# Performance work log

Hardware: AMD Instinct MI355X
Metric: run time of the kernel (lower is better)

Reference implementation:

```python
import jax, jax.numpy as jnp
import numpy as np

INF_SUB_NUM = -9000000000000000.0
LN_EPS = 1e-5


def _layernorm(x, gamma, beta):
    mu = jnp.mean(x, axis=-1, keepdims=True)
    var = jnp.mean(jnp.square(x - mu), axis=-1, keepdims=True)
    return gamma * (x - mu) * jax.lax.rsqrt(var + LN_EPS) + beta


def setup_inputs() -> dict:
    key = jax.random.key(0)
    kh, ke, kt, kw1, kw2 = jax.random.split(key, 5)
    B, N, E, D = 8, 4096, 2048, 256
    stdv = 1.0 / np.sqrt(D)
    return {
        "hidden": jax.random.normal(kh, (B, N, D), dtype=jnp.float32),
        "ht": jax.random.randint(kt, (B, E, N), 0, 2, dtype=jnp.int32),
        "edge_emb": jax.random.normal(ke, (B, E, D), dtype=jnp.float32),
        "wnk": jax.random.uniform(kw1, (D, D), jnp.float32, -stdv, stdv),
        "wek": jax.random.uniform(kw2, (D, D), jnp.float32, -stdv, stdv),
        "ln_gamma": jnp.ones((D,), jnp.float32),
        "ln_beta": jnp.zeros((D,), jnp.float32),
    }


def reference(hidden, ht, edge_emb, wnk, wek, ln_gamma, ln_beta):
    # hidden: [B,N,D]; ht: [B,E,N] incidence; edge_emb: [B,E,D]
    D = hidden.shape[-1]
    scale = 1.0 / jnp.sqrt(jnp.float32(D))

    edge_emb = _layernorm(edge_emb, ln_gamma, ln_beta)          # [B,E,D]
    node_k = hidden @ wnk                                        # [B,N,D]

    # Stage 1: edges attend over their incident nodes (softmax over N, dim=2)
    edge_scores = jnp.einsum('bed,bnd->ben', edge_emb, node_k) * scale
    edge_scores = jnp.where(ht > 0, edge_scores, INF_SUB_NUM)
    attn_edge = jax.nn.softmax(edge_scores, axis=2)              # [B,E,N]
    edge_h = jnp.einsum('ben,bnd->bed', attn_edge, hidden) + edge_emb

    # Stage 2: nodes gather from edges; softmax over N (dim=1), as in source
    edge_k = edge_h @ wek                                        # [B,E,D]
    node_scores = jnp.einsum('bnd,bed->bne', node_k, edge_k) * scale
    node_scores = jnp.where(jnp.transpose(ht, (0, 2, 1)) > 0, node_scores, INF_SUB_NUM)
    attn_node = jax.nn.softmax(node_scores, axis=1)              # [B,N,E]
    node_hidden = jnp.einsum('bne,bed->bnd', attn_node, edge_h)  # [B,N,D]
    return node_hidden
```

## Files before the change

### kernel.cpp

```cpp
#include <hip/hip_runtime.h>
#include <hip/hip_bf16.h>
#include <stdint.h>


#define B_ 8
#define N_ 4096
#define E_ 2048
#define D_ 256
#define INF_SUB (-9.0e15f)

typedef short bf16x8 __attribute__((ext_vector_type(8)));
typedef float f32x4 __attribute__((ext_vector_type(4)));
typedef unsigned short us8 __attribute__((ext_vector_type(8)));

#define AS1 __attribute__((address_space(1)))
#define AS3 __attribute__((address_space(3)))

__device__ __forceinline__ unsigned short f2bf(float f) {
    union { float f; unsigned int u; } v; v.f = f;
    unsigned int r = v.u + 0x7fffu + ((v.u >> 16) & 1u);
    return (unsigned short)(r >> 16);
}
__device__ __forceinline__ float bf2f(unsigned short h) {
    union { unsigned int u; float f; } v; v.u = ((unsigned int)h) << 16;
    return v.f;
}
__device__ __forceinline__ float waveReduceSum(float v) {
#pragma unroll
    for (int o = 32; o > 0; o >>= 1) v += __shfl_xor(v, o, 64);
    return v;
}

__global__ __launch_bounds__(256) void ln_kernel(const float* __restrict__ x,
                                                 const float* __restrict__ gamma,
                                                 const float* __restrict__ beta,
                                                 unsigned short* __restrict__ yb) {
    __shared__ float red[8];
    const int row = blockIdx.x;
    const int t = threadIdx.x;
    const int lane = t & 63, wid = t >> 6;
    const float v = x[(size_t)row * D_ + t];
    float s = waveReduceSum(v);
    if (lane == 0) red[wid] = s;
    __syncthreads();
    const float mu = (red[0] + red[1] + red[2] + red[3]) * (1.0f / D_);
    const float d = v - mu;
    float s2 = waveReduceSum(d * d);
    if (lane == 0) red[4 + wid] = s2;
    __syncthreads();
    const float var = (red[4] + red[5] + red[6] + red[7]) * (1.0f / D_);
    yb[(size_t)row * D_ + t] = f2bf(gamma[t] * d * rsqrtf(var + 1e-5f) + beta[t]);
}

__global__ __launch_bounds__(256) void pack_mask(const int* __restrict__ ht,
                                                 uint32_t* __restrict__ bits) {
    const int row = blockIdx.x;
    const int t = threadIdx.x, wid = t >> 6, lane = t & 63;
    const int* hrow = ht + (size_t)row * N_;
    uint32_t* brow = bits + (size_t)row * (N_ / 32);
#pragma unroll
    for (int i = 0; i < 16; ++i) {
        const int c = wid * 16 + i;
        const int v = hrow[c * 64 + lane];
        unsigned long long m = __ballot(v > 0);
        if (lane == 0) {
            brow[c * 2] = (uint32_t)m;
            brow[c * 2 + 1] = (uint32_t)(m >> 32);
        }
    }
}

__global__ __launch_bounds__(256) void prep_hidden(const float* __restrict__ in,
                                                   unsigned short* __restrict__ hb,
                                                   unsigned short* __restrict__ hT) {
    __shared__ unsigned short tile[64][65];
    const int b = blockIdx.z;
    in += (size_t)b * N_ * D_;
    hb += (size_t)b * N_ * D_;
    hT += (size_t)b * D_ * N_;
    const int n0 = blockIdx.y * 64, d0 = blockIdx.x * 64;
    const int t = threadIdx.x;
    const int tr = t >> 4, tc = (t & 15) * 4;
#pragma unroll
    for (int q = 0; q < 4; ++q) {
        const int rr = q * 16 + tr;
        const float4 f = *(const float4*)&in[(size_t)(n0 + rr) * D_ + d0 + tc];
        unsigned short h0 = f2bf(f.x), h1 = f2bf(f.y), h2 = f2bf(f.z), h3 = f2bf(f.w);
        *(ushort4*)&hb[(size_t)(n0 + rr) * D_ + d0 + tc] = make_ushort4(h0, h1, h2, h3);
        tile[rr][tc + 0] = h0; tile[rr][tc + 1] = h1;
        tile[rr][tc + 2] = h2; tile[rr][tc + 3] = h3;
    }
    __syncthreads();
#pragma unroll
    for (int q = 0; q < 4; ++q) {
        const int cc = q * 16 + tr;
        ushort4 o = make_ushort4(tile[tc + 0][cc], tile[tc + 1][cc],
                                 tile[tc + 2][cc], tile[tc + 3][cc]);
        *(ushort4*)&hT[(size_t)(d0 + cc) * N_ + n0 + tc] = o;
    }
}

__global__ __launch_bounds__(256) void cast_wT(const float* __restrict__ w,
                                               unsigned short* __restrict__ wT) {
    const int gid = blockIdx.x * 256 + threadIdx.x;
    const int i = gid >> 8, j = gid & 255;
    wT[j * D_ + i] = f2bf(w[i * D_ + j]);
}

__global__ __launch_bounds__(256) void reduce_pv(const float* __restrict__ slab,
                                                 const unsigned short* __restrict__ eln,
                                                 const float* __restrict__ rsum,
                                                 unsigned short* __restrict__ eh,
                                                 float* __restrict__ ehT) {
    __shared__ float tile[64][65];
    const int b = blockIdx.z;
    const float* s0 = slab + (size_t)(b * 2) * E_ * D_;
    const float* s1 = slab + (size_t)(b * 2 + 1) * E_ * D_;
    const int e0 = blockIdx.y * 64, d0 = blockIdx.x * 64;
    const int t = threadIdx.x;
    const int tr = t >> 4, tc = (t & 15) * 4;
#pragma unroll
    for (int q = 0; q < 4; ++q) {
        const int rr = q * 16 + tr;
        const int row = e0 + rr;
        const float4 v0 = *(const float4*)&s0[(size_t)row * D_ + d0 + tc];
        const float4 v1 = *(const float4*)&s1[(size_t)row * D_ + d0 + tc];
        const float inv = 1.0f / rsum[(size_t)b * E_ + row];
        const ushort4 el = *(const ushort4*)&eln[(size_t)b * E_ * D_ + (size_t)row * D_ + d0 + tc];
        const float x0 = (v0.x + v1.x) * inv + bf2f(el.x);
        const float x1 = (v0.y + v1.y) * inv + bf2f(el.y);
        const float x2 = (v0.z + v1.z) * inv + bf2f(el.z);
        const float x3 = (v0.w + v1.w) * inv + bf2f(el.w);
        *(ushort4*)&eh[(size_t)b * E_ * D_ + (size_t)row * D_ + d0 + tc] =
            make_ushort4(f2bf(x0), f2bf(x1), f2bf(x2), f2bf(x3));
        tile[rr][tc + 0] = x0; tile[rr][tc + 1] = x1;
        tile[rr][tc + 2] = x2; tile[rr][tc + 3] = x3;
    }
    __syncthreads();
#pragma unroll
    for (int q = 0; q < 4; ++q) {
        const int cc = q * 16 + tr;
        float4 o = make_float4(tile[tc + 0][cc], tile[tc + 1][cc],
                               tile[tc + 2][cc], tile[tc + 3][cc]);
        *(float4*)&ehT[(size_t)b * D_ * E_ + (size_t)(d0 + cc) * E_ + e0 + tc] = o;
    }
}

__global__ __launch_bounds__(256) void scale_ehT(const float* __restrict__ ehT,
                                                 const float* __restrict__ lsum,
                                                 unsigned short* __restrict__ ehs) {
    const size_t base = ((size_t)blockIdx.x * 256 + threadIdx.x) * 8;
    const int b = (int)(base / ((size_t)D_ * E_));
    const int e = (int)(base % E_);
    const float4 f0 = *(const float4*)&ehT[base];
    const float4 f1 = *(const float4*)&ehT[base + 4];
    const float4 l0 = *(const float4*)&lsum[(size_t)b * E_ + e];
    const float4 l1 = *(const float4*)&lsum[(size_t)b * E_ + e + 4];
    us8 o;
    o[0] = f2bf(f0.x / l0.x); o[1] = f2bf(f0.y / l0.y);
    o[2] = f2bf(f0.z / l0.z); o[3] = f2bf(f0.w / l0.w);
    o[4] = f2bf(f1.x / l1.x); o[5] = f2bf(f1.y / l1.y);
    o[6] = f2bf(f1.z / l1.z); o[7] = f2bf(f1.w / l1.w);
    *(us8*)&ehs[base] = o;
}

#define M_BF16 0
#define M_MASK 1
#define M_F32 2

template <int MODE, int MASKOR, int AEXP, int ASUM, int SPLIT, int CSUM>
__global__ __launch_bounds__(256) void mfma_gemm_nt(
        const short* __restrict__ A, const short* __restrict__ Bm,
        void* __restrict__ Cv, const uint32_t* __restrict__ bits,
        float* __restrict__ sums,
        int K, int ldc, size_t sA, size_t sB, size_t sC, float scale) {
    __shared__ __align__(16) short ls[(MODE == M_F32) ? 16384 : 16896];
    __shared__ uint32_t mwords[MASKOR ? 512 : 4];
    short* lsA = ls;
    short* lsB = ls + 8192;
    const int zb = blockIdx.z;
    const int b = SPLIT ? (zb >> 1) : zb;
    A += (size_t)b * sA;
    Bm += (size_t)b * sB;
    const int m0 = blockIdx.y * 128, n0 = blockIdx.x * 128;
    const int tid = threadIdx.x, wid = tid >> 6, lane = tid & 63;
    const int l15 = lane & 15, kg = lane >> 4;
    const int wr = wid >> 1, wc = wid & 1;

    if (MASKOR) {
        const uint32_t* bb = bits + (size_t)b * E_ * (N_ / 32);
#pragma unroll
        for (int q = 0; q < 2; ++q) {
            const int idx = q * 256 + tid;
            mwords[idx] = (MASKOR == 1)
                ? bb[(size_t)(m0 + (idx >> 2)) * (N_ / 32) + (n0 >> 5) + (idx & 3)]
                : bb[(size_t)(n0 + (idx >> 2)) * (N_ / 32) + (m0 >> 5) + (idx & 3)];
        }
    }

    int raoff[4], rota[4], rboff[4], rotb[4];
#pragma unroll
    for (int i = 0; i < 4; ++i) {
        const int ra = wr * 64 + i * 16 + l15;
        raoff[i] = ra * 64; rota[i] = kg + (ra >> 1);
        const int rb = wc * 64 + i * 16 + l15;
        rboff[i] = rb * 64; rotb[i] = kg + (rb >> 1);
    }
    const f32x4 zero = {0.f, 0.f, 0.f, 0.f};
    f32x4 acc[4][4];
#pragma unroll
    for (int i = 0; i < 4; ++i)
#pragma unroll
        for (int j = 0; j < 4; ++j) acc[i][j] = zero;

    float rsumLoc = 0.f;
    const int ar = tid >> 1, ah = tid & 1;

    const int kt0 = SPLIT ? (zb & 1) * (K >> 1) : 0;
    const int ktE = SPLIT ? kt0 + (K >> 1) : K;
    for (int kt = kt0; kt < ktE; kt += 64) {
        __syncthreads();
        if (AEXP) {
            const short* ga = A + (size_t)(m0 + ar) * K + kt + ah * 32;
            us8 raw[4], ex[4];
#pragma unroll
            for (int c = 0; c < 4; ++c) raw[c] = *(const us8*)(ga + c * 8);
#pragma unroll
            for (int c = 0; c < 4; ++c)
#pragma unroll
                for (int j = 0; j < 8; ++j) {
                    const float x = __expf(bf2f(raw[c][j]));
                    if (ASUM) rsumLoc += x;
                    ex[c][j] = f2bf(x);
                }
#pragma unroll
            for (int c = 0; c < 4; ++c) {
                const int p = (ah * 4 + c + (ar >> 1)) & 7;
                *(us8*)&lsA[ar * 64 + p * 8] = ex[c];
            }
#pragma unroll
            for (int q = 0; q < 4; ++q) {
                const int c = q * 256 + tid;
                const int r = c >> 3;
                const int kc = ((c & 7) - (r >> 1)) & 7;
                const short* gb = Bm + (size_t)(n0 + r) * K + kt + kc * 8;
                __builtin_amdgcn_global_load_lds((const AS1 void*)gb,
                    (AS3 void*)(lsB + (q * 256 + wid * 64) * 8), 16, 0, 0);
            }
        } else {
#pragma unroll
            for (int q = 0; q < 4; ++q) {
                const int c = q * 256 + tid;
                const int r = c >> 3;
                const int kc = ((c & 7) - (r >> 1)) & 7;
                const short* ga = A + (size_t)(m0 + r) * K + kt + kc * 8;
                __builtin_amdgcn_global_load_lds((const AS1 void*)ga,
                    (AS3 void*)(lsA + (q * 256 + wid * 64) * 8), 16, 0, 0);
                const short* gb = Bm + (size_t)(n0 + r) * K + kt + kc * 8;
                __builtin_amdgcn_global_load_lds((const AS1 void*)gb,
                    (AS3 void*)(lsB + (q * 256 + wid * 64) * 8), 16, 0, 0);
            }
        }
        __syncthreads();
#pragma unroll
        for (int s = 0; s < 2; ++s) {
            bf16x8 fa[4], fb[4];
#pragma unroll
            for (int i = 0; i < 4; ++i)
                fa[i] = *(const bf16x8*)(lsA + raoff[i] + (((s * 4 + rota[i]) & 7) << 3));
#pragma unroll
            for (int j = 0; j < 4; ++j)
                fb[j] = *(const bf16x8*)(lsB + rboff[j] + (((s * 4 + rotb[j]) & 7) << 3));
#pragma unroll
            for (int i = 0; i < 4; ++i)
#pragma unroll
                for (int j = 0; j < 4; ++j)
                    acc[i][j] = __builtin_amdgcn_mfma_f32_16x16x32_bf16(fa[i], fb[j], acc[i][j], 0, 0, 0);
        }
    }

    if (AEXP && ASUM) {
        const float tot = rsumLoc + __shfl_xor(rsumLoc, 1, 64);
        if (ah == 0 && blockIdx.x == 0)
            atomicAdd(&sums[(size_t)b * E_ + m0 + ar], tot);
    }

    __syncthreads();

    if (MODE == M_F32) {
        float* C = (float*)Cv + (SPLIT ? (size_t)zb * sC : (size_t)b * sC);
        float* lsF = (float*)ls;
#pragma unroll
        for (int h = 0; h < 4; ++h) {
            if (wr == (h >> 1)) {
#pragma unroll
                for (int ii = 0; ii < 2; ++ii) {
                    const int i = (h & 1) * 2 + ii;
#pragma unroll
                    for (int j = 0; j < 4; ++j)
#pragma unroll
                        for (int r = 0; r < 4; ++r) {
                            const int rl = ii * 16 + kg * 4 + r;
                            const int cl = wc * 64 + j * 16 + l15;
                            lsF[rl * 128 + cl] = acc[i][j][r];
                        }
                }
            }
            __syncthreads();
#pragma unroll
            for (int si = 0; si < 4; ++si) {
                const int row = (tid >> 5) + si * 8;
                const int colb = (tid & 31) * 4;
                float4 v = *(float4*)&lsF[row * 128 + colb];
                *(float4*)&C[(size_t)(m0 + h * 32 + row) * ldc + n0 + colb] = v;
            }
            __syncthreads();
        }
    } else {
        unsigned short* C = (unsigned short*)Cv + (size_t)b * sC;
        float evsum[4] = {0.f, 0.f, 0.f, 0.f};
#pragma unroll
        for (int i = 0; i < 4; ++i) {
#pragma unroll
            for (int r = 0; r < 4; ++r) {
                const int rowfull = wr * 64 + i * 16 + kg * 4 + r;
                uint64_t mwr = 0;
                if (MODE == M_MASK && MASKOR == 1)
                    mwr = *(const uint64_t*)&mwords[rowfull * 4 + wc * 2];
#pragma unroll
                for (int j = 0; j < 4; ++j) {
                    const int cl = wc * 64 + j * 16 + l15;
                    float v = acc[i][j][r];
                    if (MODE == M_MASK) {
                        v *= scale;
                        uint32_t bit;
                        if (MASKOR == 1) {
                            bit = (uint32_t)(mwr >> (j * 16 + l15)) & 1u;
                        } else {
                            const uint64_t mwc = *(const uint64_t*)&mwords[cl * 4 + wr * 2];
                            bit = (uint32_t)(mwc >> (i * 16 + kg * 4 + r)) & 1u;
                        }
                        if (!bit) v = INF_SUB;
                    }
                    ls[rowfull * 132 + cl] = (short)f2bf(v);
                    if (CSUM) evsum[j] += __expf(v);
                }
            }
        }
        __syncthreads();
#pragma unroll
        for (int si = 0; si < 8; ++si) {
            const int row = (tid >> 4) + si * 16;
            const int col = (tid & 15) * 8;
            us8 val = *(us8*)&ls[row * 132 + col];
            *(us8*)&C[(size_t)(m0 + row) * ldc + n0 + col] = val;
        }
        if (CSUM) {
#pragma unroll
            for (int j = 0; j < 4; ++j) {
                float cs = evsum[j];
                cs += __shfl_xor(cs, 16, 64);
                cs += __shfl_xor(cs, 32, 64);
                if (kg == 0)
                    atomicAdd(&sums[(size_t)b * E_ + n0 + wc * 64 + j * 16 + l15], cs);
            }
        }
    }
}

extern "C" void kernel_launch(void* const* d_in, const int* in_sizes, int n_in,
                              void* d_out, int out_size, void* d_ws, size_t ws_size,
                              hipStream_t stream) {
    const float* hidden = (const float*)d_in[0];
    const int* ht = (const int*)d_in[1];
    const float* edge_emb = (const float*)d_in[2];
    const float* wnk = (const float*)d_in[3];
    const float* wek = (const float*)d_in[4];
    const float* gamma = (const float*)d_in[5];
    const float* beta = (const float*)d_in[6];
    float* out = (float*)d_out;
    (void)in_sizes; (void)n_in; (void)out_size; (void)ws_size;

    char* w = (char*)d_ws;
    unsigned short* SP = (unsigned short*)w;         w += (size_t)B_ * E_ * N_ * 2;
    unsigned short* hidden_bf = (unsigned short*)w;  w += (size_t)B_ * N_ * D_ * 2;
    unsigned short* hiddenT_bf = (unsigned short*)w; w += (size_t)B_ * D_ * N_ * 2;
    unsigned short* node_k_bf = (unsigned short*)w;  w += (size_t)B_ * N_ * D_ * 2;
    unsigned short* eln_bf = (unsigned short*)w;     w += (size_t)B_ * E_ * D_ * 2;
    unsigned short* edge_h_bf = (unsigned short*)w;  w += (size_t)B_ * E_ * D_ * 2;
    float* ehT_f32 = (float*)w;                      w += (size_t)B_ * D_ * E_ * 4;
    unsigned short* ehsT_bf = (unsigned short*)w;    w += (size_t)B_ * D_ * E_ * 2;
    unsigned short* edge_k_bf = (unsigned short*)w;  w += (size_t)B_ * E_ * D_ * 2;
    float* slabs = (float*)w;                        w += (size_t)B_ * 2 * E_ * D_ * 4;
    uint32_t* bits = (uint32_t*)w;                   w += (size_t)B_ * E_ * (N_ / 32) * 4;
    float* rsum = (float*)w;                         w += (size_t)B_ * E_ * 4;
    float* lsum = (float*)w;                         w += (size_t)B_ * E_ * 4;
    unsigned short* wnkT = (unsigned short*)w;       w += (size_t)D_ * D_ * 2;
    unsigned short* wekT = (unsigned short*)w;       w += (size_t)D_ * D_ * 2;

    const float scale = 0.0625f;

    prep_hidden<<<dim3(D_ / 64, N_ / 64, B_), 256, 0, stream>>>(hidden, hidden_bf, hiddenT_bf);
    cast_wT<<<D_ * D_ / 256, 256, 0, stream>>>(wnk, wnkT);
    cast_wT<<<D_ * D_ / 256, 256, 0, stream>>>(wek, wekT);
    ln_kernel<<<B_ * E_, 256, 0, stream>>>(edge_emb, gamma, beta, eln_bf);
    pack_mask<<<B_ * E_, 256, 0, stream>>>(ht, bits);
    hipMemsetAsync(rsum, 0, (size_t)B_ * E_ * 8, stream);

    mfma_gemm_nt<M_BF16, 0, 0, 0, 0, 0><<<dim3(D_ / 128, (B_ * N_) / 128, 1), 256, 0, stream>>>(
        (const short*)hidden_bf, (const short*)wnkT, node_k_bf, nullptr, nullptr,
        D_, D_, 0, 0, 0, 1.f);
    mfma_gemm_nt<M_MASK, 1, 0, 0, 0, 0><<<dim3(N_ / 128, E_ / 128, B_), 256, 0, stream>>>(
        (const short*)eln_bf, (const short*)node_k_bf, SP, bits, nullptr,
        D_, N_, (size_t)E_ * D_, (size_t)N_ * D_, (size_t)E_ * N_, scale);
    mfma_gemm_nt<M_F32, 0, 1, 1, 1, 0><<<dim3(D_ / 128, E_ / 128, B_ * 2), 256, 0, stream>>>(
        (const short*)SP, (const short*)hiddenT_bf, slabs, nullptr, rsum,
        N_, D_, (size_t)E_ * N_, (size_t)D_ * N_, (size_t)E_ * D_, 1.f);
    reduce_pv<<<dim3(D_ / 64, E_ / 64, B_), 256, 0, stream>>>(
        slabs, eln_bf, rsum, edge_h_bf, ehT_f32);
    mfma_gemm_nt<M_BF16, 0, 0, 0, 0, 0><<<dim3(D_ / 128, (B_ * E_) / 128, 1), 256, 0, stream>>>(
        (const short*)edge_h_bf, (const short*)wekT, edge_k_bf, nullptr, nullptr,
        D_, D_, 0, 0, 0, 1.f);
    mfma_gemm_nt<M_MASK, 2, 0, 0, 0, 1><<<dim3(E_ / 128, N_ / 128, B_), 256, 0, stream>>>(
        (const short*)node_k_bf, (const short*)edge_k_bf, SP, bits, lsum,
        D_, E_, (size_t)N_ * D_, (size_t)E_ * D_, (size_t)N_ * E_, scale);
    scale_ehT<<<(B_ * D_ * E_) / (256 * 8), 256, 0, stream>>>(ehT_f32, lsum, ehsT_bf);
    mfma_gemm_nt<M_F32, 0, 1, 0, 0, 0><<<dim3(D_ / 128, N_ / 128, B_), 256, 0, stream>>>(
        (const short*)SP, (const short*)ehsT_bf, out, nullptr, nullptr,
        E_, D_, (size_t)N_ * E_, (size_t)D_ * E_, (size_t)N_ * D_, 1.f);
}
```

Before: 790.3 us.

## Move softmax exp and row sums into score GEMM epilogue

```diff
diff --git a/kernel.cpp b/kernel.cpp
--- a/kernel.cpp
+++ b/kernel.cpp
@@ -168,7 +168,7 @@
 #define M_MASK 1
 #define M_F32 2
 
-template <int MODE, int MASKOR, int AEXP, int ASUM, int SPLIT, int CSUM>
+template <int MODE, int MASKOR, int RSUM, int SPLIT, int CSUM>
 __global__ __launch_bounds__(256) void mfma_gemm_nt(
         const short* __restrict__ A, const short* __restrict__ Bm,
         void* __restrict__ Cv, const uint32_t* __restrict__ bits,
@@ -213,53 +213,21 @@
 #pragma unroll
         for (int j = 0; j < 4; ++j) acc[i][j] = zero;
 
-    float rsumLoc = 0.f;
-    const int ar = tid >> 1, ah = tid & 1;
-
     const int kt0 = SPLIT ? (zb & 1) * (K >> 1) : 0;
     const int ktE = SPLIT ? kt0 + (K >> 1) : K;
     for (int kt = kt0; kt < ktE; kt += 64) {
         __syncthreads();
-        if (AEXP) {
-            const short* ga = A + (size_t)(m0 + ar) * K + kt + ah * 32;
-            us8 raw[4], ex[4];
-#pragma unroll
-            for (int c = 0; c < 4; ++c) raw[c] = *(const us8*)(ga + c * 8);
-#pragma unroll
-            for (int c = 0; c < 4; ++c)
-#pragma unroll
-                for (int j = 0; j < 8; ++j) {
-                    const float x = __expf(bf2f(raw[c][j]));
-                    if (ASUM) rsumLoc += x;
-                    ex[c][j] = f2bf(x);
-                }
-#pragma unroll
-            for (int c = 0; c < 4; ++c) {
-                const int p = (ah * 4 + c + (ar >> 1)) & 7;
-                *(us8*)&lsA[ar * 64 + p * 8] = ex[c];
-            }
-#pragma unroll
-            for (int q = 0; q < 4; ++q) {
-                const int c = q * 256 + tid;
-                const int r = c >> 3;
-                const int kc = ((c & 7) - (r >> 1)) & 7;
-                const short* gb = Bm + (size_t)(n0 + r) * K + kt + kc * 8;
-                __builtin_amdgcn_global_load_lds((const AS1 void*)gb,
-                    (AS3 void*)(lsB + (q * 256 + wid * 64) * 8), 16, 0, 0);
-            }
-        } else {
-#pragma unroll
-            for (int q = 0; q < 4; ++q) {
-                const int c = q * 256 + tid;
-                const int r = c >> 3;
-                const int kc = ((c & 7) - (r >> 1)) & 7;
-                const short* ga = A + (size_t)(m0 + r) * K + kt + kc * 8;
-                __builtin_amdgcn_global_load_lds((const AS1 void*)ga,
-                    (AS3 void*)(lsA + (q * 256 + wid * 64) * 8), 16, 0, 0);
-                const short* gb = Bm + (size_t)(n0 + r) * K + kt + kc * 8;
-                __builtin_amdgcn_global_load_lds((const AS1 void*)gb,
-                    (AS3 void*)(lsB + (q * 256 + wid * 64) * 8), 16, 0, 0);
-            }
+#pragma unroll
+        for (int q = 0; q < 4; ++q) {
+            const int c = q * 256 + tid;
+            const int r = c >> 3;
+            const int kc = ((c & 7) - (r >> 1)) & 7;
+            const short* ga = A + (size_t)(m0 + r) * K + kt + kc * 8;
+            __builtin_amdgcn_global_load_lds((const AS1 void*)ga,
+                (AS3 void*)(lsA + (q * 256 + wid * 64) * 8), 16, 0, 0);
+            const short* gb = Bm + (size_t)(n0 + r) * K + kt + kc * 8;
+            __builtin_amdgcn_global_load_lds((const AS1 void*)gb,
+                (AS3 void*)(lsB + (q * 256 + wid * 64) * 8), 16, 0, 0);
         }
         __syncthreads();
 #pragma unroll
@@ -277,12 +245,6 @@
                 for (int j = 0; j < 4; ++j)
                     acc[i][j] = __builtin_amdgcn_mfma_f32_16x16x32_bf16(fa[i], fb[j], acc[i][j], 0, 0, 0);
         }
-    }
-
-    if (AEXP && ASUM) {
-        const float tot = rsumLoc + __shfl_xor(rsumLoc, 1, 64);
-        if (ah == 0 && blockIdx.x == 0)
-            atomicAdd(&sums[(size_t)b * E_ + m0 + ar], tot);
     }
 
     __syncthreads();
@@ -327,6 +289,7 @@
                 uint64_t mwr = 0;
                 if (MODE == M_MASK && MASKOR == 1)
                     mwr = *(const uint64_t*)&mwords[rowfull * 4 + wc * 2];
+                float rs = 0.f;
 #pragma unroll
                 for (int j = 0; j < 4; ++j) {
                     const int cl = wc * 64 + j * 16 + l15;
@@ -340,10 +303,19 @@
                             const uint64_t mwc = *(const uint64_t*)&mwords[cl * 4 + wr * 2];
                             bit = (uint32_t)(mwc >> (i * 16 + kg * 4 + r)) & 1u;
                         }
-                        if (!bit) v = INF_SUB;
+                        v = bit ? __expf(v) : 0.f;
+                        if (CSUM) evsum[j] += v;
+                        if (RSUM) rs += v;
                     }
                     ls[rowfull * 132 + cl] = (short)f2bf(v);
-                    if (CSUM) evsum[j] += __expf(v);
+                }
+                if (RSUM) {
+                    rs += __shfl_xor(rs, 1, 64);
+                    rs += __shfl_xor(rs, 2, 64);
+                    rs += __shfl_xor(rs, 4, 64);
+                    rs += __shfl_xor(rs, 8, 64);
+                    if (l15 == 0)
+                        atomicAdd(&sums[(size_t)b * E_ + m0 + rowfull], rs);
                 }
             }
         }
@@ -407,25 +379,25 @@
     pack_mask<<<B_ * E_, 256, 0, stream>>>(ht, bits);
     hipMemsetAsync(rsum, 0, (size_t)B_ * E_ * 8, stream);
 
-    mfma_gemm_nt<M_BF16, 0, 0, 0, 0, 0><<<dim3(D_ / 128, (B_ * N_) / 128, 1), 256, 0, stream>>>(
+    mfma_gemm_nt<M_BF16, 0, 0, 0, 0><<<dim3(D_ / 128, (B_ * N_) / 128, 1), 256, 0, stream>>>(
         (const short*)hidden_bf, (const short*)wnkT, node_k_bf, nullptr, nullptr,
         D_, D_, 0, 0, 0, 1.f);
-    mfma_gemm_nt<M_MASK, 1, 0, 0, 0, 0><<<dim3(N_ / 128, E_ / 128, B_), 256, 0, stream>>>(
-        (const short*)eln_bf, (const short*)node_k_bf, SP, bits, nullptr,
+    mfma_gemm_nt<M_MASK, 1, 1, 0, 0><<<dim3(N_ / 128, E_ / 128, B_), 256, 0, stream>>>(
+        (const short*)eln_bf, (const short*)node_k_bf, SP, bits, rsum,
         D_, N_, (size_t)E_ * D_, (size_t)N_ * D_, (size_t)E_ * N_, scale);
-    mfma_gemm_nt<M_F32, 0, 1, 1, 1, 0><<<dim3(D_ / 128, E_ / 128, B_ * 2), 256, 0, stream>>>(
-        (const short*)SP, (const short*)hiddenT_bf, slabs, nullptr, rsum,
+    mfma_gemm_nt<M_F32, 0, 0, 1, 0><<<dim3(D_ / 128, E_ / 128, B_ * 2), 256, 0, stream>>>(
+        (const short*)SP, (const short*)hiddenT_bf, slabs, nullptr, nullptr,
         N_, D_, (size_t)E_ * N_, (size_t)D_ * N_, (size_t)E_ * D_, 1.f);
     reduce_pv<<<dim3(D_ / 64, E_ / 64, B_), 256, 0, stream>>>(
         slabs, eln_bf, rsum, edge_h_bf, ehT_f32);
-    mfma_gemm_nt<M_BF16, 0, 0, 0, 0, 0><<<dim3(D_ / 128, (B_ * E_) / 128, 1), 256, 0, stream>>>(
+    mfma_gemm_nt<M_BF16, 0, 0, 0, 0><<<dim3(D_ / 128, (B_ * E_) / 128, 1), 256, 0, stream>>>(
         (const short*)edge_h_bf, (const short*)wekT, edge_k_bf, nullptr, nullptr,
         D_, D_, 0, 0, 0, 1.f);
-    mfma_gemm_nt<M_MASK, 2, 0, 0, 0, 1><<<dim3(E_ / 128, N_ / 128, B_), 256, 0, stream>>>(
+    mfma_gemm_nt<M_MASK, 2, 0, 0, 1><<<dim3(E_ / 128, N_ / 128, B_), 256, 0, stream>>>(
         (const short*)node_k_bf, (const short*)edge_k_bf, SP, bits, lsum,
         D_, E_, (size_t)N_ * D_, (size_t)E_ * D_, (size_t)N_ * E_, scale);
     scale_ehT<<<(B_ * D_ * E_) / (256 * 8), 256, 0, stream>>>(ehT_f32, lsum, ehsT_bf);
-    mfma_gemm_nt<M_F32, 0, 1, 0, 0, 0><<<dim3(D_ / 128, N_ / 128, B_), 256, 0, stream>>>(
+    mfma_gemm_nt<M_F32, 0, 0, 0, 0><<<dim3(D_ / 128, N_ / 128, B_), 256, 0, stream>>>(
         (const short*)SP, (const short*)ehsT_bf, out, nullptr, nullptr,
         E_, D_, (size_t)N_ * E_, (size_t)D_ * E_, (size_t)N_ * D_, 1.f);
 }
```

Result: faster. 772.8 us (-2.2%).
